# Performance work log

Measured on AMD Instinct MI355X. Metric: run time of the kernel, lower is better.

The kernel has to match this reference:

```python
import jax, jax.numpy as jnp
import numpy as np

WINDOW_SIZE = 11
SIGMA = 1.5
C1 = 0.01 ** 2
C2 = 0.03 ** 2


def _gaussian_window(window_size=WINDOW_SIZE, sigma=SIGMA):
    coords = jnp.arange(window_size, dtype=jnp.float32) - window_size // 2
    g = jnp.exp(-(coords ** 2) / (2.0 * sigma ** 2))
    g = g / g.sum()
    w3d = g[:, None, None] * g[None, :, None] * g[None, None, :]
    w3d = w3d / w3d.sum()
    return w3d[None, None]  # [1, 1, K, K, K] (OIDHW)


def _gconv3d(x, window):
    # depthwise 3D conv, SAME padding (pad = K//2), groups = C
    C = x.shape[1]
    w = jnp.broadcast_to(window, (C, 1) + window.shape[2:])
    pad = window.shape[-1] // 2
    return jax.lax.conv_general_dilated(
        x, w,
        window_strides=(1, 1, 1),
        padding=[(pad, pad)] * 3,
        dimension_numbers=("NCDHW", "OIDHW", "NCDHW"),
        feature_group_count=C,
    )


def setup_inputs() -> dict:
    key = jax.random.key(0)
    k1, k2 = jax.random.split(key)
    shape = (4, 1, 64, 192, 192)  # [B, C, D, H, W]
    pred = jax.random.uniform(k1, shape, dtype=jnp.float32)
    target = jax.random.uniform(k2, shape, dtype=jnp.float32)
    return {"pred": pred, "target": target}


def reference(pred, target):
    window = _gaussian_window()
    mu_p = _gconv3d(pred, window)
    mu_t = _gconv3d(target, window)
    mu_p_sq = mu_p ** 2
    mu_t_sq = mu_t ** 2
    mu_pt = mu_p * mu_t
    sigma_p_sq = _gconv3d(pred ** 2, window) - mu_p_sq
    sigma_t_sq = _gconv3d(target ** 2, window) - mu_t_sq
    sigma_pt = _gconv3d(pred * target, window) - mu_pt
    ssim_map = ((2.0 * mu_pt + C1) * (2.0 * sigma_pt + C2)) / (
        (mu_p_sq + mu_t_sq + C1) * (sigma_p_sq + sigma_t_sq + C2)
    )
    return 1.0 - ssim_map.mean()
```

## Files before the change

### kernel.cpp

```cpp
#include <hip/hip_runtime.h>


#define D_DIM 64
#define H_DIM 192
#define W_DIM 192
#define SLICE (H_DIM * W_DIM)
#define VOL   (D_DIM * SLICE)
#define NB    4
#define KS    11
#define RAD   5
#define TIL   16
#define HLO   26
#define SROWS 32
#define SP2   28
#define IPP   17
#define C1F   (0.01f * 0.01f)
#define C2F   (0.03f * 0.03f)

typedef float f32x2 __attribute__((ext_vector_type(2)));

#define BAR_LDS() do {                                                    \
    asm volatile("s_waitcnt lgkmcnt(0)" ::: "memory");                    \
    __builtin_amdgcn_s_barrier();                                         \
    __builtin_amdgcn_sched_barrier(0);                                    \
} while (0)

__device__ __forceinline__ void make_window(float* g) {
    float s = 0.f;
#pragma unroll
    for (int i = 0; i < KS; ++i) {
        float c = (float)(i - RAD);
        g[i] = expf(-(c * c) * (1.0f / 4.5f));
        s += g[i];
    }
    float inv = 1.0f / s;
#pragma unroll
    for (int i = 0; i < KS; ++i) g[i] *= inv;
}

#define SSIM_ACC(MP, MT, E2, T2, PT) do {                                 \
    float _mps = (MP) * (MP), _mts = (MT) * (MT), _mpt = (MP) * (MT);     \
    float _num = (2.f * _mpt + C1F) * (2.f * ((PT) - _mpt) + C2F);        \
    float _den = (_mps + _mts + C1F) *                                    \
                 (((E2) - _mps) + ((T2) - _mts) + C2F);                   \
    ssim_sum += _num * __builtin_amdgcn_rcpf(_den);                       \
} while (0)

__global__ __launch_bounds__(256) void fused_ssim_kernel(
    const float* __restrict__ pred, const float* __restrict__ targ,
    float* __restrict__ partials) {
    __shared__ f32x2 spt[SROWS * SP2];
    __shared__ f32x2 i01[SROWS * IPP];
    __shared__ f32x2 i23[SROWS * IPP];
    __shared__ float i4 [SROWS * IPP];
    __shared__ float red[4];

    float g[KS];
    make_window(g);

    const int tid = threadIdx.x;
    const int h0 = (blockIdx.x / 12) * TIL;
    const int w0 = (blockIdx.x % 12) * TIL;
    const int half = blockIdx.y;
    const float* pb = pred + (size_t)blockIdx.z * VOL;
    const float* tb = targ + (size_t)blockIdx.z * VOL;
    const int q0 = half ? 27 : 0;
    const int q1 = half ? 63 : 36;
    const int d_lo = half ? 32 : 0;
    const int d_hi = half ? 63 : 31;

    for (int i = HLO * SP2 + tid; i < SROWS * SP2; i += 256)
        spt[i] = (f32x2){0.f, 0.f};

    int sidx[3], slds[3];
    bool sa[3], sv[3];
#pragma unroll
    for (int k = 0; k < 3; ++k) {
        int i = tid + 256 * k;
        sa[k] = i < HLO * HLO;
        int y = i / HLO, x = i - y * HLO;
        int gh = h0 + y - RAD, gw = w0 + x - RAD;
        sv[k] = sa[k] && (unsigned)gh < (unsigned)H_DIM &&
                (unsigned)gw < (unsigned)W_DIM;
        sidx[k] = gh * W_DIM + gw;
        slds[k] = y * SP2 + x;
    }
    const int py = tid >> 4, px = tid & 15;

    f32x2 a01[KS], a23[KS];
    float a4[KS];
#pragma unroll
    for (int j = 0; j < KS; ++j) {
        a01[j] = (f32x2){0.f, 0.f};
        a23[j] = (f32x2){0.f, 0.f};
        a4[j] = 0.f;
    }
    float ssim_sum = 0.f;

    float rp[3], rt[3];
    {
        const float* pq = pb + q0 * SLICE;
        const float* tq = tb + q0 * SLICE;
#pragma unroll
        for (int k = 0; k < 3; ++k) {
            rp[k] = sv[k] ? pq[sidx[k]] : 0.f;
            rt[k] = sv[k] ? tq[sidx[k]] : 0.f;
        }
    }

    for (int q = q0;; ++q) {
#pragma unroll
        for (int k = 0; k < 3; ++k)
            if (sa[k]) spt[slds[k]] = (f32x2){rp[k], rt[k]};
        if (q < q1) {
            const float* pn = pb + (q + 1) * SLICE;
            const float* tn = tb + (q + 1) * SLICE;
#pragma unroll
            for (int k = 0; k < 3; ++k) {
                rp[k] = sv[k] ? pn[sidx[k]] : 0.f;
                rt[k] = sv[k] ? tn[sidx[k]] : 0.f;
            }
        }
        BAR_LDS();

#pragma unroll
        for (int it = 0; it < 2; ++it) {
            int t = tid + it * 256;
            int r = t >> 4, c = t & 15;
            const f32x2* pr = spt + r * SP2 + c;
            f32x2 s01 = (f32x2){0.f, 0.f};
            f32x2 s23 = (f32x2){0.f, 0.f};
            float s4 = 0.f;
#pragma unroll
            for (int k = 0; k < KS; ++k) {
                f32x2 v = pr[k];
                float gk = g[k];
                f32x2 gk2 = (f32x2){gk, gk};
                s01 += gk2 * v;
                s23 += gk2 * (v * v);
                s4 += gk * (v.x * v.y);
            }
            int oi = r * IPP + c;
            i01[oi] = s01;
            i23[oi] = s23;
            i4 [oi] = s4;
        }
        BAR_LDS();

        {
            const f32x2* c01 = i01 + px;
            const f32x2* c23 = i23 + px;
            const float* c4  = i4  + px;
            f32x2 v01 = (f32x2){0.f, 0.f};
            f32x2 v23 = (f32x2){0.f, 0.f};
            float v4 = 0.f;
#pragma unroll
            for (int k = 0; k < KS; ++k) {
                int rr = (py + k) * IPP;
                float gk = g[k];
                f32x2 gk2 = (f32x2){gk, gk};
                v01 += gk2 * c01[rr];
                v23 += gk2 * c23[rr];
                v4 += gk * c4[rr];
            }
#pragma unroll
            for (int j = 0; j < KS; ++j) {
                float wj = g[10 - j];
                f32x2 wj2 = (f32x2){wj, wj};
                a01[j] += wj2 * v01;
                a23[j] += wj2 * v23;
                a4[j] += wj * v4;
            }
            if (q - 5 >= d_lo)
                SSIM_ACC(a01[0].x, a01[0].y, a23[0].x, a23[0].y, a4[0]);
#pragma unroll
            for (int j = 0; j < KS - 1; ++j) {
                a01[j] = a01[j + 1]; a23[j] = a23[j + 1]; a4[j] = a4[j + 1];
            }
            a01[10] = (f32x2){0.f, 0.f};
            a23[10] = (f32x2){0.f, 0.f};
            a4[10] = 0.f;
        }
        if (q == q1) break;
    }

#pragma unroll
    for (int j = 0; j < 5; ++j) {
        int d = q1 - 4 + j;
        if (d >= d_lo && d <= d_hi)
            SSIM_ACC(a01[j].x, a01[j].y, a23[j].x, a23[j].y, a4[j]);
    }

    float a = ssim_sum;
#pragma unroll
    for (int off = 32; off > 0; off >>= 1) a += __shfl_down(a, off, 64);
    int lane = tid & 63, wv = tid >> 6;
    if (lane == 0) red[wv] = a;
    __syncthreads();
    if (tid == 0)
        partials[((blockIdx.z * 2 + blockIdx.y) * 144) + blockIdx.x] =
            red[0] + red[1] + red[2] + red[3];
}

__global__ __launch_bounds__(256) void finalize_kernel(
    const float* __restrict__ partials, int n, float* __restrict__ out) {
    double a = 0.0;
    for (int i = threadIdx.x; i < n; i += 256) a += (double)partials[i];
#pragma unroll
    for (int off = 32; off > 0; off >>= 1) a += __shfl_down(a, off, 64);
    __shared__ double red[4];
    int lane = threadIdx.x & 63, wv = threadIdx.x >> 6;
    if (lane == 0) red[wv] = a;
    __syncthreads();
    if (threadIdx.x == 0) {
        double s = red[0] + red[1] + red[2] + red[3];
        out[0] = (float)(1.0 - s / (double)((long long)NB * VOL));
    }
}

extern "C" void kernel_launch(void* const* d_in, const int* in_sizes, int n_in,
                              void* d_out, int out_size, void* d_ws, size_t ws_size,
                              hipStream_t stream) {
    const float* pred = (const float*)d_in[0];
    const float* targ = (const float*)d_in[1];
    float* out = (float*)d_out;
    float* partials = (float*)d_ws;

    fused_ssim_kernel<<<dim3(144, 2, NB), 256, 0, stream>>>(pred, targ, partials);
    finalize_kernel<<<1, 256, 0, stream>>>(partials, NB * 288, out);
}
```

Baseline: 203.3 us.

## Software-pipeline depth slices with double-buffered LDS and one barrier per step

Result: no change. 201.4 us (-0.9%).

```diff
diff --git a/kernel.cpp b/kernel.cpp
--- a/kernel.cpp
+++ b/kernel.cpp
@@ -14,6 +14,7 @@
 #define SROWS 32
 #define SP2   28
 #define IPP   17
+#define NPL   36
 #define C1F   (0.01f * 0.01f)
 #define C2F   (0.03f * 0.03f)
 
@@ -46,13 +47,93 @@
     ssim_sum += _num * __builtin_amdgcn_rcpf(_den);                       \
 } while (0)
 
+#define CM(i) do {                                                        \
+    f32x2* _s = Sb[(i) & 1];                                              \
+    _Pragma("unroll")                                                     \
+    for (int _k = 0; _k < 3; ++_k)                                        \
+        if (sa[_k]) _s[slds[_k]] = (f32x2){rp[_k], rt[_k]};               \
+} while (0)
+
+#define PF(i) do {                                                        \
+    const float* _pn = pb + (q0 + (i) + 1) * SLICE;                       \
+    const float* _tn = tb + (q0 + (i) + 1) * SLICE;                       \
+    _Pragma("unroll")                                                     \
+    for (int _k = 0; _k < 3; ++_k) {                                      \
+        rp[_k] = sv[_k] ? _pn[sidx[_k]] : 0.f;                            \
+        rt[_k] = sv[_k] ? _tn[sidx[_k]] : 0.f;                            \
+    }                                                                     \
+} while (0)
+
+#define WPH(i) do {                                                       \
+    const int _b = ((i) - 1) & 1;                                         \
+    const f32x2* _sp = Sb[_b];                                            \
+    _Pragma("unroll")                                                     \
+    for (int _it = 0; _it < 2; ++_it) {                                   \
+        int _t = tid + _it * 256;                                         \
+        int _r = _t >> 4, _c = _t & 15;                                   \
+        const f32x2* _pr = _sp + _r * SP2 + _c;                           \
+        f32x2 _s01 = (f32x2){0.f, 0.f};                                   \
+        f32x2 _s23 = (f32x2){0.f, 0.f};                                   \
+        float _s4 = 0.f;                                                  \
+        _Pragma("unroll")                                                 \
+        for (int _k = 0; _k < KS; ++_k) {                                 \
+            f32x2 _v = _pr[_k];                                           \
+            float _gk = g[_k];                                            \
+            f32x2 _g2 = (f32x2){_gk, _gk};                                \
+            _s01 += _g2 * _v;                                             \
+            _s23 += _g2 * (_v * _v);                                      \
+            _s4 += _gk * (_v.x * _v.y);                                   \
+        }                                                                 \
+        int _oi = _r * IPP + _c;                                          \
+        I01b[_b][_oi] = _s01;                                             \
+        I23b[_b][_oi] = _s23;                                             \
+        I4b [_b][_oi] = _s4;                                              \
+    }                                                                     \
+} while (0)
+
+#define HPH(i) do {                                                       \
+    const int _b = (i) & 1;                                               \
+    const f32x2* _c01 = I01b[_b] + px;                                    \
+    const f32x2* _c23 = I23b[_b] + px;                                    \
+    const float* _c4  = I4b [_b] + px;                                    \
+    f32x2 _v01 = (f32x2){0.f, 0.f};                                       \
+    f32x2 _v23 = (f32x2){0.f, 0.f};                                       \
+    float _v4 = 0.f;                                                      \
+    _Pragma("unroll")                                                     \
+    for (int _k = 0; _k < KS; ++_k) {                                     \
+        int _rr = (py + _k) * IPP;                                        \
+        float _gk = g[_k];                                                \
+        f32x2 _g2 = (f32x2){_gk, _gk};                                    \
+        _v01 += _g2 * _c01[_rr];                                          \
+        _v23 += _g2 * _c23[_rr];                                          \
+        _v4 += _gk * _c4[_rr];                                            \
+    }                                                                     \
+    _Pragma("unroll")                                                     \
+    for (int _j = 0; _j < KS; ++_j) {                                     \
+        float _wj = g[10 - _j];                                           \
+        f32x2 _w2 = (f32x2){_wj, _wj};                                    \
+        a01[_j] += _w2 * _v01;                                            \
+        a23[_j] += _w2 * _v23;                                            \
+        a4[_j] += _wj * _v4;                                              \
+    }                                                                     \
+    if (q0 + (i) - 7 >= d_lo)                                             \
+        SSIM_ACC(a01[0].x, a01[0].y, a23[0].x, a23[0].y, a4[0]);          \
+    _Pragma("unroll")                                                     \
+    for (int _j = 0; _j < KS - 1; ++_j) {                                 \
+        a01[_j] = a01[_j + 1]; a23[_j] = a23[_j + 1]; a4[_j] = a4[_j + 1];\
+    }                                                                     \
+    a01[10] = (f32x2){0.f, 0.f};                                          \
+    a23[10] = (f32x2){0.f, 0.f};                                          \
+    a4[10] = 0.f;                                                         \
+} while (0)
+
 __global__ __launch_bounds__(256) void fused_ssim_kernel(
     const float* __restrict__ pred, const float* __restrict__ targ,
     float* __restrict__ partials) {
-    __shared__ f32x2 spt[SROWS * SP2];
-    __shared__ f32x2 i01[SROWS * IPP];
-    __shared__ f32x2 i23[SROWS * IPP];
-    __shared__ float i4 [SROWS * IPP];
+    __shared__ f32x2 Sb[2][SROWS * SP2];
+    __shared__ f32x2 I01b[2][SROWS * IPP];
+    __shared__ f32x2 I23b[2][SROWS * IPP];
+    __shared__ float I4b[2][SROWS * IPP];
     __shared__ float red[4];
 
     float g[KS];
@@ -65,12 +146,13 @@
     const float* pb = pred + (size_t)blockIdx.z * VOL;
     const float* tb = targ + (size_t)blockIdx.z * VOL;
     const int q0 = half ? 27 : 0;
-    const int q1 = half ? 63 : 36;
     const int d_lo = half ? 32 : 0;
     const int d_hi = half ? 63 : 31;
 
-    for (int i = HLO * SP2 + tid; i < SROWS * SP2; i += 256)
-        spt[i] = (f32x2){0.f, 0.f};
+    for (int i = HLO * SP2 + tid; i < SROWS * SP2; i += 256) {
+        Sb[0][i] = (f32x2){0.f, 0.f};
+        Sb[1][i] = (f32x2){0.f, 0.f};
+    }
 
     int sidx[3], slds[3];
     bool sa[3], sv[3];
@@ -108,85 +190,18 @@
         }
     }
 
-    for (int q = q0;; ++q) {
-#pragma unroll
-        for (int k = 0; k < 3; ++k)
-            if (sa[k]) spt[slds[k]] = (f32x2){rp[k], rt[k]};
-        if (q < q1) {
-            const float* pn = pb + (q + 1) * SLICE;
-            const float* tn = tb + (q + 1) * SLICE;
-#pragma unroll
-            for (int k = 0; k < 3; ++k) {
-                rp[k] = sv[k] ? pn[sidx[k]] : 0.f;
-                rt[k] = sv[k] ? tn[sidx[k]] : 0.f;
-            }
-        }
-        BAR_LDS();
-
-#pragma unroll
-        for (int it = 0; it < 2; ++it) {
-            int t = tid + it * 256;
-            int r = t >> 4, c = t & 15;
-            const f32x2* pr = spt + r * SP2 + c;
-            f32x2 s01 = (f32x2){0.f, 0.f};
-            f32x2 s23 = (f32x2){0.f, 0.f};
-            float s4 = 0.f;
-#pragma unroll
-            for (int k = 0; k < KS; ++k) {
-                f32x2 v = pr[k];
-                float gk = g[k];
-                f32x2 gk2 = (f32x2){gk, gk};
-                s01 += gk2 * v;
-                s23 += gk2 * (v * v);
-                s4 += gk * (v.x * v.y);
-            }
-            int oi = r * IPP + c;
-            i01[oi] = s01;
-            i23[oi] = s23;
-            i4 [oi] = s4;
-        }
-        BAR_LDS();
-
-        {
-            const f32x2* c01 = i01 + px;
-            const f32x2* c23 = i23 + px;
-            const float* c4  = i4  + px;
-            f32x2 v01 = (f32x2){0.f, 0.f};
-            f32x2 v23 = (f32x2){0.f, 0.f};
-            float v4 = 0.f;
-#pragma unroll
-            for (int k = 0; k < KS; ++k) {
-                int rr = (py + k) * IPP;
-                float gk = g[k];
-                f32x2 gk2 = (f32x2){gk, gk};
-                v01 += gk2 * c01[rr];
-                v23 += gk2 * c23[rr];
-                v4 += gk * c4[rr];
-            }
-#pragma unroll
-            for (int j = 0; j < KS; ++j) {
-                float wj = g[10 - j];
-                f32x2 wj2 = (f32x2){wj, wj};
-                a01[j] += wj2 * v01;
-                a23[j] += wj2 * v23;
-                a4[j] += wj * v4;
-            }
-            if (q - 5 >= d_lo)
-                SSIM_ACC(a01[0].x, a01[0].y, a23[0].x, a23[0].y, a4[0]);
-#pragma unroll
-            for (int j = 0; j < KS - 1; ++j) {
-                a01[j] = a01[j + 1]; a23[j] = a23[j + 1]; a4[j] = a4[j + 1];
-            }
-            a01[10] = (f32x2){0.f, 0.f};
-            a23[10] = (f32x2){0.f, 0.f};
-            a4[10] = 0.f;
-        }
-        if (q == q1) break;
-    }
+    CM(0); PF(0); BAR_LDS();
+    CM(1); PF(1); WPH(1); BAR_LDS();
+    for (int i = 2; i <= NPL - 1; ++i) {
+        CM(i); PF(i); WPH(i); HPH(i); BAR_LDS();
+    }
+    CM(NPL); WPH(NPL); HPH(NPL); BAR_LDS();
+    WPH(NPL + 1); HPH(NPL + 1); BAR_LDS();
+    HPH(NPL + 2);
 
 #pragma unroll
     for (int j = 0; j < 5; ++j) {
-        int d = q1 - 4 + j;
+        int d = q0 + NPL - 4 + j;
         if (d >= d_lo && d <= d_hi)
             SSIM_ACC(a01[j].x, a01[j].y, a23[j].x, a23[j].y, a4[j]);
     }
```
